# Kernel optimization log

Measured on AMD Instinct MI355X. Metric: run time of the kernel, lower is better.

## Reference

```python
import jax, jax.numpy as jnp
import numpy as np

KERNEL = 31  # median window size (librosa HPSS default)
POWER = 2.0
MARGIN = 1.0


def _median_last(x, k):
    # median filter along the last axis with zero padding ((k-1)//2 each side),
    # matching F.conv2d one-hot unfold + torch.median in the original.
    pad = (k - 1) // 2
    xp = jnp.pad(x, ((0, 0), (0, 0), (0, 0), (pad, pad)))
    W = x.shape[-1]
    # [B,C,H,W,k] sliding windows (k is a small fixed constant -> loop ok)
    windows = jnp.stack([xp[..., i:i + W] for i in range(k)], axis=-1)
    return jnp.median(windows, axis=-1)


def _median_freq(x, k):
    # median filter along the H (freq) axis
    pad = (k - 1) // 2
    xp = jnp.pad(x, ((0, 0), (0, 0), (pad, pad), (0, 0)))
    H = x.shape[-2]
    windows = jnp.stack([xp[..., i:i + H, :] for i in range(k)], axis=-1)
    return jnp.median(windows, axis=-1)


def _softmask(X, X_ref, power):
    tiny = jnp.finfo(X.dtype).tiny
    Z = jnp.maximum(X, X_ref)
    Z = jnp.where(Z < tiny, jnp.ones_like(Z), Z)
    m = (X / Z) ** power
    r = (X_ref / Z) ** power
    return m / (m + r)


def setup_inputs() -> dict:
    key = jax.random.key(0)
    S = jax.random.uniform(key, (2, 2, 1025, 1024), dtype=jnp.float32)
    return {"S": S}


def reference(S):
    # harmonic: median along time (kernel (1,31)); percussive: along freq (kernel (31,1))
    harm = _median_last(S, KERNEL)
    perc = _median_freq(S, KERNEL)
    mask_harm = _softmask(harm, perc * MARGIN, POWER)
    mask_perc = _softmask(perc, harm * MARGIN, POWER)
    return (S * mask_harm, S * mask_perc)
```

## Files before the change

### kernel.cpp

```cpp
#include <hip/hip_runtime.h>

#define BC 4
#define HD 1025
#define WD 1024
#define KWIN 31
#define HCH 16
#define PCH 8
#define REG 1056

__device__ __forceinline__ void ce(float& x, float& y) {
    float lo = fminf(x, y);
    float hi = fmaxf(x, y);
    x = lo; y = hi;
}

__device__ __forceinline__ void sort31(float* a) {
#pragma unroll
    for (int pk = 4; pk >= 0; --pk) {
        const int p = 1 << pk;
#pragma unroll
        for (int k = 0; k <= 4 - pk; ++k) {
            const int d = (k == 0) ? p : ((16 >> (k - 1)) - p);
            const int r = (k == 0) ? 0 : p;
#pragma unroll
            for (int i = 0; i < KWIN - d; ++i)
                if ((i & p) == r) ce(a[i], a[i + d]);
        }
    }
}

__device__ __forceinline__ float slide_med(float* win, float oldv, float newv) {
    float rp = (win[0] >= oldv) ? win[1] : win[0];
    win[0] = fminf(rp, newv);
#pragma unroll
    for (int i = 1; i < KWIN - 1; ++i) {
        float rc = (win[i] >= oldv) ? win[i + 1] : win[i];
        win[i] = __builtin_amdgcn_fmed3f(newv, rp, rc);
        rp = rc;
    }
    win[KWIN - 1] = fmaxf(newv, rp);
    return win[15];
}

__device__ __forceinline__ float* swz(float* base, int f ) {
    int u = f >> 2;
    u ^= (u >> 3) & 7;
    return base + (u << 2);
}

__global__ __launch_bounds__(256, 4) void harm_kernel(const float* __restrict__ S,
                                                      float* __restrict__ harm) {
    __shared__ float lds[4 * REG];
    const int tid = threadIdx.x;
    const int wv = tid >> 6, ln = tid & 63;
    const int row = blockIdx.x * 4 + wv;
    const int plane = blockIdx.z;
    const bool rowok = (row < HD);
    float* wl = lds + wv * REG;
    const float* rowg = S + ((size_t)plane * HD + row) * WD;

    if (rowok) {
#pragma unroll
        for (int it = 0; it < 5; ++it) {
            int t = 4 * ln + 256 * it;
            if (t < REG) {
                int g = t - 16;
                float4 v;
                if (g >= 0 && g + 3 < WD) {
                    v = *(const float4*)(rowg + g);
                } else {
                    v.x = ((unsigned)(g + 0) < WD) ? rowg[g + 0] : 0.f;
                    v.y = ((unsigned)(g + 1) < WD) ? rowg[g + 1] : 0.f;
                    v.z = ((unsigned)(g + 2) < WD) ? rowg[g + 2] : 0.f;
                    v.w = ((unsigned)(g + 3) < WD) ? rowg[g + 3] : 0.f;
                }
                *(float4*)swz(wl, t) = v;
            }
        }
    }
    __builtin_amdgcn_wave_barrier();

    float m[HCH];
    if (rowok) {
        float raw[48];
#pragma unroll
        for (int k = 0; k < 12; ++k) {
            float4 v = *(const float4*)swz(wl, 16 * ln + 4 * k);
            raw[4 * k + 0] = v.x; raw[4 * k + 1] = v.y;
            raw[4 * k + 2] = v.z; raw[4 * k + 3] = v.w;
        }
        float win[KWIN];
#pragma unroll
        for (int j = 0; j < KWIN; ++j) win[j] = raw[1 + j];
        sort31(win);
        m[0] = win[15];
#pragma unroll
        for (int s = 1; s < HCH; ++s)
            m[s] = slide_med(win, raw[s] , raw[s + 31] );
    }
    __builtin_amdgcn_wave_barrier();
    if (rowok) {
#pragma unroll
        for (int g = 0; g < 4; ++g)
            *(float4*)swz(wl, 16 * ln + 4 * g) =
                make_float4(m[4 * g + 0], m[4 * g + 1], m[4 * g + 2], m[4 * g + 3]);
    }
    __builtin_amdgcn_wave_barrier();
    if (rowok) {
        float* hrow = harm + ((size_t)plane * HD + row) * WD;
#pragma unroll
        for (int it = 0; it < 4; ++it) {
            int t = 4 * ln + 256 * it;
            *(float4*)(hrow + t) = *(const float4*)swz(wl, t);
        }
    }
}

__global__ __launch_bounds__(256, 4) void perc_mask_kernel(const float* __restrict__ S,
                                                           const float* __restrict__ harm,
                                                           float* __restrict__ out0,
                                                           float* __restrict__ out1) {
    const int w = blockIdx.x * 256 + threadIdx.x;
    const int h0 = blockIdx.y * PCH;
    const int plane = blockIdx.z;
    const size_t poff = (size_t)plane * HD * WD;
    const float* base = S + poff;

    float span[38];
#pragma unroll
    for (int j = 0; j < 38; ++j) {
        int h = h0 - 15 + j;
        span[j] = ((unsigned)h < (unsigned)HD) ? base[(size_t)h * WD + w] : 0.f;
    }

    float win[KWIN];
#pragma unroll
    for (int j = 0; j < KWIN; ++j) win[j] = span[j];
    sort31(win);

#pragma unroll
    for (int s = 0; s < PCH; ++s) {
        int h = h0 + s;
        if (h >= HD) break;
        float pm = (s == 0) ? win[15] : slide_med(win, span[s - 1], span[s + 30]);
        float sv = span[15 + s];
        size_t idx = poff + (size_t)h * WD + w;
        float hmv = harm[idx];
        float h2 = hmv * hmv;
        float p2 = pm * pm;
        float inv = 1.0f / (h2 + p2);
        out0[idx] = sv * h2 * inv;
        out1[idx] = sv * p2 * inv;
    }
}

extern "C" void kernel_launch(void* const* d_in, const int* in_sizes, int n_in,
                              void* d_out, int out_size, void* d_ws, size_t ws_size,
                              hipStream_t stream) {
    const float* S = (const float*)d_in[0];
    float* out = (float*)d_out;
    const size_t N = (size_t)BC * HD * WD;
    float* harm = out;
    float* out1 = out + N;

    dim3 hgrid((HD + 3) / 4, 1, BC);
    harm_kernel<<<hgrid, 256, 0, stream>>>(S, harm);

    dim3 pgrid(WD / 256, (HD + PCH - 1) / PCH, BC);
    perc_mask_kernel<<<pgrid, 256, 0, stream>>>(S, harm, out, out1);
}
```

Baseline: 100.5 us.

## Compute sliding medians by merging a sorted shared core with a small sliding window

Replaces the 31-element sorted-window update per output with a split approach. For each group of 8 outputs, the 24 shared elements are sorted once and a 7-element window is slid, and the median is picked with a merge-style rank-16 selection using max/min. The aim is to cut the per-output compare-exchange work from about 30 med3 operations to about 6 plus a small selection network. The cost is an extra 24-element sort per chunk and higher register use. Correctness depends on the rank-16 selection formula being right.

```diff
diff --git a/kernel.cpp b/kernel.cpp
--- a/kernel.cpp
+++ b/kernel.cpp
@@ -3,7 +3,6 @@
 #define BC 4
 #define HD 1025
 #define WD 1024
-#define KWIN 31
 #define HCH 16
 #define PCH 8
 #define REG 1056
@@ -14,32 +13,50 @@
     x = lo; y = hi;
 }
 
-__device__ __forceinline__ void sort31(float* a) {
-#pragma unroll
-    for (int pk = 4; pk >= 0; --pk) {
+template<int N, int T>
+__device__ __forceinline__ void sortN(float* a) {
+#pragma unroll
+    for (int pk = T - 1; pk >= 0; --pk) {
         const int p = 1 << pk;
 #pragma unroll
-        for (int k = 0; k <= 4 - pk; ++k) {
-            const int d = (k == 0) ? p : ((16 >> (k - 1)) - p);
+        for (int k = 0; k <= T - 1 - pk; ++k) {
+            const int d = (k == 0) ? p : (((1 << (T - 1)) >> (k - 1)) - p);
             const int r = (k == 0) ? 0 : p;
 #pragma unroll
-            for (int i = 0; i < KWIN - d; ++i)
+            for (int i = 0; i < N - d; ++i)
                 if ((i & p) == r) ce(a[i], a[i + d]);
         }
     }
 }
 
-__device__ __forceinline__ float slide_med(float* win, float oldv, float newv) {
-    float rp = (win[0] >= oldv) ? win[1] : win[0];
-    win[0] = fminf(rp, newv);
-#pragma unroll
-    for (int i = 1; i < KWIN - 1; ++i) {
-        float rc = (win[i] >= oldv) ? win[i + 1] : win[i];
-        win[i] = __builtin_amdgcn_fmed3f(newv, rp, rc);
-        rp = rc;
-    }
-    win[KWIN - 1] = fmaxf(newv, rp);
-    return win[15];
+__device__ __forceinline__ void slide7(float* M, float oldv, float newv) {
+    float r0 = (M[0] >= oldv) ? M[1] : M[0];
+    float r1 = (M[1] >= oldv) ? M[2] : M[1];
+    float r2 = (M[2] >= oldv) ? M[3] : M[2];
+    float r3 = (M[3] >= oldv) ? M[4] : M[3];
+    float r4 = (M[4] >= oldv) ? M[5] : M[4];
+    float r5 = (M[5] >= oldv) ? M[6] : M[5];
+    M[0] = fminf(r0, newv);
+    M[1] = __builtin_amdgcn_fmed3f(newv, r0, r1);
+    M[2] = __builtin_amdgcn_fmed3f(newv, r1, r2);
+    M[3] = __builtin_amdgcn_fmed3f(newv, r2, r3);
+    M[4] = __builtin_amdgcn_fmed3f(newv, r3, r4);
+    M[5] = fmaxf(r5, newv) == r5 ? __builtin_amdgcn_fmed3f(newv, r4, r5) : __builtin_amdgcn_fmed3f(newv, r4, r5);
+    M[6] = fmaxf(r5, newv);
+}
+
+__device__ __forceinline__ float sel16(const float* C, const float* M) {
+    float c0 = fmaxf(C[8],  M[6]);
+    float c1 = fmaxf(C[9],  M[5]);
+    float c2 = fmaxf(C[10], M[4]);
+    float c3 = fmaxf(C[11], M[3]);
+    float c4 = fmaxf(C[12], M[2]);
+    float c5 = fmaxf(C[13], M[1]);
+    float c6 = fmaxf(C[14], M[0]);
+    float c7 = C[15];
+    float t0 = fminf(c0, c1), t1 = fminf(c2, c3);
+    float t2 = fminf(c4, c5), t3 = fminf(c6, c7);
+    return fminf(fminf(t0, t1), fminf(t2, t3));
 }
 
 __device__ __forceinline__ float* swz(float* base, int f ) {
@@ -89,14 +106,23 @@
             raw[4 * k + 0] = v.x; raw[4 * k + 1] = v.y;
             raw[4 * k + 2] = v.z; raw[4 * k + 3] = v.w;
         }
-        float win[KWIN];
-#pragma unroll
-        for (int j = 0; j < KWIN; ++j) win[j] = raw[1 + j];
-        sort31(win);
-        m[0] = win[15];
-#pragma unroll
-        for (int s = 1; s < HCH; ++s)
-            m[s] = slide_med(win, raw[s] , raw[s + 31] );
+#pragma unroll
+        for (int c = 0; c < 2; ++c) {
+            float C[24];
+#pragma unroll
+            for (int j = 0; j < 24; ++j) C[j] = raw[8 * c + 8 + j];
+            sortN<24, 5>(C);
+            float M[7];
+#pragma unroll
+            for (int j = 0; j < 7; ++j) M[j] = raw[8 * c + 1 + j];
+            sortN<7, 3>(M);
+            m[8 * c] = sel16(C, M);
+#pragma unroll
+            for (int s = 1; s < 8; ++s) {
+                slide7(M, raw[8 * c + s], raw[8 * c + 31 + s]);
+                m[8 * c + s] = sel16(C, M);
+            }
+        }
     }
     __builtin_amdgcn_wave_barrier();
     if (rowok) {
@@ -133,16 +159,21 @@
         span[j] = ((unsigned)h < (unsigned)HD) ? base[(size_t)h * WD + w] : 0.f;
     }
 
-    float win[KWIN];
-#pragma unroll
-    for (int j = 0; j < KWIN; ++j) win[j] = span[j];
-    sort31(win);
+    float C[24];
+#pragma unroll
+    for (int j = 0; j < 24; ++j) C[j] = span[7 + j];
+    sortN<24, 5>(C);
+    float M[7];
+#pragma unroll
+    for (int j = 0; j < 7; ++j) M[j] = span[j];
+    sortN<7, 3>(M);
 
 #pragma unroll
     for (int s = 0; s < PCH; ++s) {
         int h = h0 + s;
         if (h >= HD) break;
-        float pm = (s == 0) ? win[15] : slide_med(win, span[s - 1], span[s + 30]);
+        if (s > 0) slide7(M, span[s - 1], span[s + 30]);
+        float pm = sel16(C, M);
         float sv = span[15 + s];
         size_t idx = poff + (size_t)h * WD + w;
         float hmv = harm[idx];
```

New measurement: 97.90 us. 1.03x faster.
